# Performance work log

Hardware: AMD Instinct MI355X
Metric: run time of the kernel (lower is better)

The kernel has to match this reference:

```python
import jax, jax.numpy as jnp
import numpy as np

NEG_INF = -1e9  # stands in for the -inf diagonal mask of criss-cross attention
BN_EPS = 1e-5


def conv1x1(x, w, b=None):
    # x: [B,Cin,H,W], w: [Cout,Cin]
    y = jnp.einsum('bchw,oc->bohw', x, w)
    if b is not None:
        y = y + b[None, :, None, None]
    return y


def criss_cross(qf, kf, vf, q_w, q_b, k_w, k_b, v_w, v_b, gamma):
    # Criss-cross attention (CCNet): row + column affinity, joint softmax, aggregate.
    B, C, H, W = vf.shape
    q = conv1x1(qf, q_w, q_b)  # [B,Ci,H,W]
    k = conv1x1(kf, k_w, k_b)  # [B,Ci,H,W]
    v = conv1x1(vf, v_w, v_b)  # [B,C,H,W]
    # column-wise (along H) energy, with -inf on the self position (h == h')
    eH = jnp.einsum('bchw,bcHw->bhwH', q, k)
    eH = eH + NEG_INF * jnp.eye(H, dtype=eH.dtype)[:, None, :]  # [H,1,H] broadcasts over w
    # row-wise (along W) energy
    eW = jnp.einsum('bchw,bchW->bhwW', q, k)
    att = jax.nn.softmax(jnp.concatenate([eH, eW], axis=-1), axis=-1)  # [B,H,W,H+W]
    aH, aW = att[..., :H], att[..., H:]
    outH = jnp.einsum('bcHw,bhwH->bchw', v, aH)
    outW = jnp.einsum('bchW,bhwW->bchw', v, aW)
    return gamma * (outH + outW) + vf


def batchnorm(x, scale, bias):
    # training-mode BN over (N,H,W)
    mean = x.mean(axis=(0, 2, 3), keepdims=True)
    var = x.var(axis=(0, 2, 3), keepdims=True)
    xh = (x - mean) * jax.lax.rsqrt(var + BN_EPS)
    return xh * scale[None, :, None, None] + bias[None, :, None, None]


def setup_inputs() -> dict:
    key = jax.random.key(0)
    ks = jax.random.split(key, 16)
    B, C, H, W = 8, 512, 96, 96
    Hh, Wh = 48, 48
    Cin = C // 2    # 256
    Ci = C // 16    # 32
    s = 0.02
    inp = {
        'low_feature': jax.random.normal(ks[0], (B, C, H, W), jnp.float32),
        'high_feature': jax.random.normal(ks[1], (B, C, Hh, Wh), jnp.float32),
        'conv1_w': jax.random.normal(ks[2], (Cin, C), jnp.float32) * s,
        'conv1_b': jnp.zeros((Cin,), jnp.float32),
        'conv2_w': jax.random.normal(ks[3], (Cin, C), jnp.float32) * s,
        'conv2_b': jnp.zeros((Cin,), jnp.float32),
        'q_w': jax.random.normal(ks[4], (Ci, Cin), jnp.float32) * s,
        'q_b': jnp.zeros((Ci,), jnp.float32),
        'k_w': jax.random.normal(ks[5], (Ci, Cin), jnp.float32) * s,
        'k_b': jnp.zeros((Ci,), jnp.float32),
        'v_w': jax.random.normal(ks[6], (Cin, Cin), jnp.float32) * s,
        'v_b': jnp.zeros((Cin,), jnp.float32),
        'gamma': jnp.array(0.1, jnp.float32),
        'bottleneck_w': jax.random.normal(ks[7], (C, Cin + C), jnp.float32) * s,
        'bn_scale': jnp.ones((C,), jnp.float32),
        'bn_bias': jnp.zeros((C,), jnp.float32),
    }
    return inp


def reference(low_feature, high_feature, conv1_w, conv1_b, conv2_w, conv2_b,
              q_w, q_b, k_w, k_b, v_w, v_b, gamma, bottleneck_w, bn_scale, bn_bias):
    B, C, H, W = low_feature.shape
    hf = jax.image.resize(high_feature, (B, high_feature.shape[1], H, W), method='bilinear')
    qf = conv1x1(low_feature, conv1_w, conv1_b)   # [B,C/2,H,W]
    vf = conv1x1(hf, conv2_w, conv2_b)            # [B,C/2,H,W]
    for _ in range(2):  # module applies the same attention twice
        vf = criss_cross(qf, vf, vf, q_w, q_b, k_w, k_b, v_w, v_b, gamma)
    cat = jnp.concatenate([vf, hf], axis=1)       # [B, C/2 + C, H, W]
    out = conv1x1(cat, bottleneck_w)              # bias=False
    out = batchnorm(out, bn_scale, bn_bias)
    return jax.nn.relu(out)
```

## Files before the change

kernel.cpp:

```cpp
#include <hip/hip_runtime.h>
#include <hip/hip_bf16.h>

typedef __hip_bfloat16 bf16;
typedef __attribute__((ext_vector_type(8))) short short8;
typedef __attribute__((ext_vector_type(4))) float f32x4;

constexpr int kHW = 96 * 96;

__device__ __forceinline__ float b2f(bf16 x){ return __bfloat162float(x); }
__device__ __forceinline__ bf16  f2b(float x){ return __float2bfloat16(x); }

__global__ void k_zero(float* __restrict__ p){
  int i = blockIdx.x*256 + threadIdx.x;
  if (i < 1024) p[i] = 0.0f;
}

__global__ void k_cvt(const float* __restrict__ s, bf16* __restrict__ d, int n){
  int i = blockIdx.x*256 + threadIdx.x;
  if (i < n) d[i] = f2b(s[i]);
}

__global__ __launch_bounds__(256) void k_upsample(const float* __restrict__ hi,
                                                  bf16* __restrict__ hf_t){
  int y = blockIdx.x, b = blockIdx.y, t = threadIdx.x;
  int j = y >> 1;
  int j0, j1; float wy0, wy1;
  if ((y & 1) == 0){ j0 = j - 1; if (j0 < 0) j0 = 0; j1 = j; wy0 = 0.25f; wy1 = 0.75f; }
  else             { j0 = j; j1 = j + 1; if (j1 > 47) j1 = 47; wy0 = 0.75f; wy1 = 0.25f; }
  __shared__ __align__(16) float sm[2][128][49];
  for (int c0 = 0; c0 < 512; c0 += 128){
    for (int e = t; e < 2*128*48; e += 256){
      int cl = e / 96; int r = e % 96; int jj = r / 48; int i = r % 48;
      int row = jj ? j1 : j0;
      sm[jj][cl][i] = hi[(((size_t)b*512 + c0 + cl)*48 + row)*48 + i];
    }
    __syncthreads();
    for (int e = t; e < 96*128; e += 256){
      int x = e >> 7; int cl = e & 127;
      int i = x >> 1; int i0, i1; float wx0, wx1;
      if ((x & 1) == 0){ i0 = i - 1; if (i0 < 0) i0 = 0; i1 = i; wx0 = 0.25f; wx1 = 0.75f; }
      else             { i0 = i; i1 = i + 1; if (i1 > 47) i1 = 47; wx0 = 0.75f; wx1 = 0.25f; }
      float v = wy0*(wx0*sm[0][cl][i0] + wx1*sm[0][cl][i1])
              + wy1*(wx0*sm[1][cl][i0] + wx1*sm[1][cl][i1]);
      hf_t[(((size_t)b*96 + x)*96 + y)*512 + c0 + cl] = f2b(v);
    }
    __syncthreads();
  }
}

__global__ void k_qqw(const float* __restrict__ q_w, const float* __restrict__ c1_w,
                      float* __restrict__ qq_w){
  int gid = blockIdx.x*256 + threadIdx.x;
  int o = gid >> 9, c = gid & 511;
  float acc = 0.f;
  for (int k = 0; k < 256; k++) acc += q_w[o*256 + k] * c1_w[k*512 + c];
  qq_w[gid] = acc;
}
__global__ void k_qqb(const float* __restrict__ q_w, const float* __restrict__ c1_b,
                      const float* __restrict__ q_b, float* __restrict__ qq_b){
  int o = threadIdx.x; if (o >= 32) return;
  float acc = q_b[o];
  for (int k = 0; k < 256; k++) acc += q_w[o*256 + k] * c1_b[k];
  qq_b[o] = acc;
}

__global__ __launch_bounds__(256) void k_mfma_gemm(const bf16* __restrict__ A,
                                                   const bf16* __restrict__ Wb,
                                                   const float* __restrict__ bias,
                                                   bf16* __restrict__ out,
                                                   int K, int O){
  int b = blockIdx.z, n0 = blockIdx.x*128, o0 = blockIdx.y*128;
  int t = threadIdx.x, lane = t & 63, wv = t >> 6;
  int m_off = (wv & 1)*64, o_off = (wv >> 1)*64;
  int lm = lane & 15, lk = lane >> 4;
  __shared__ __align__(16) bf16 As[128*40];
  __shared__ __align__(16) bf16 Ws[128*40];
  f32x4 acc[4][4] = {};
  const bf16* Ab = A + (size_t)b*kHW*K;
  for (int c0 = 0; c0 < K; c0 += 32){
    for (int e = t; e < 512; e += 256){
      int nl = e >> 2, p = e & 3;
      *(uint4*)&As[nl*40 + p*8] = *(const uint4*)&Ab[(size_t)(n0+nl)*K + c0 + p*8];
    }
    for (int e = t; e < 512; e += 256){
      int ol = e >> 2, p = e & 3;
      *(uint4*)&Ws[ol*40 + p*8] = *(const uint4*)&Wb[(size_t)(o0+ol)*K + c0 + p*8];
    }
    __syncthreads();
    short8 af[4], bfr[4];
    #pragma unroll
    for (int i = 0; i < 4; i++){
      af[i]  = *(const short8*)&As[(m_off + i*16 + lm)*40 + lk*8];
      bfr[i] = *(const short8*)&Ws[(o_off + i*16 + lm)*40 + lk*8];
    }
    #pragma unroll
    for (int i = 0; i < 4; i++)
      #pragma unroll
      for (int j = 0; j < 4; j++)
        acc[i][j] = __builtin_amdgcn_mfma_f32_16x16x32_bf16(af[i], bfr[j], acc[i][j], 0, 0, 0);
    __syncthreads();
  }
  #pragma unroll
  for (int j = 0; j < 4; j++){
    int oc = o0 + o_off + j*16 + lm;
    float bs = bias ? bias[oc] : 0.0f;
    #pragma unroll
    for (int i = 0; i < 4; i++){
      int rbase = n0 + m_off + i*16 + lk*4;
      #pragma unroll
      for (int r = 0; r < 4; r++)
        out[((size_t)b*kHW + rbase + r)*(size_t)O + oc] = f2b(acc[i][j][r] + bs);
    }
  }
}

__global__ __launch_bounds__(256) void k_bneck_mfma(const bf16* __restrict__ vf,
                                                    const bf16* __restrict__ hf,
                                                    const bf16* __restrict__ Wb,
                                                    bf16* __restrict__ out){
  int b = blockIdx.z, n0 = blockIdx.x*128, o0 = blockIdx.y*128;
  int t = threadIdx.x, lane = t & 63, wv = t >> 6;
  int m_off = (wv & 1)*64, o_off = (wv >> 1)*64;
  int lm = lane & 15, lk = lane >> 4;
  __shared__ __align__(16) bf16 As[128*40];
  __shared__ __align__(16) bf16 Ws[128*40];
  f32x4 acc[4][4] = {};
  for (int c0 = 0; c0 < 768; c0 += 32){
    const bf16* src; int strd, cc;
    if (c0 < 256){ src = vf + (size_t)b*kHW*256; strd = 256; cc = c0; }
    else         { src = hf + (size_t)b*kHW*512; strd = 512; cc = c0 - 256; }
    for (int e = t; e < 512; e += 256){
      int nl = e >> 2, p = e & 3;
      *(uint4*)&As[nl*40 + p*8] = *(const uint4*)&src[(size_t)(n0+nl)*strd + cc + p*8];
    }
    for (int e = t; e < 512; e += 256){
      int ol = e >> 2, p = e & 3;
      *(uint4*)&Ws[ol*40 + p*8] = *(const uint4*)&Wb[(size_t)(o0+ol)*768 + c0 + p*8];
    }
    __syncthreads();
    short8 af[4], bfr[4];
    #pragma unroll
    for (int i = 0; i < 4; i++){
      af[i]  = *(const short8*)&As[(m_off + i*16 + lm)*40 + lk*8];
      bfr[i] = *(const short8*)&Ws[(o_off + i*16 + lm)*40 + lk*8];
    }
    #pragma unroll
    for (int i = 0; i < 4; i++)
      #pragma unroll
      for (int j = 0; j < 4; j++)
        acc[i][j] = __builtin_amdgcn_mfma_f32_16x16x32_bf16(af[i], bfr[j], acc[i][j], 0, 0, 0);
    __syncthreads();
  }
  #pragma unroll
  for (int j = 0; j < 4; j++){
    int oc = o0 + o_off + j*16 + lm;
    #pragma unroll
    for (int i = 0; i < 4; i++){
      int rbase = n0 + m_off + i*16 + lk*4;
      #pragma unroll
      for (int r = 0; r < 4; r++)
        out[((size_t)b*kHW + rbase + r)*512 + oc] = f2b(acc[i][j][r]);
    }
  }
}

__global__ __launch_bounds__(256) void k_stats(const bf16* __restrict__ bt,
                                               float* __restrict__ s1,
                                               float* __restrict__ s2){
  int n0 = blockIdx.x*256, b = blockIdx.y, t = threadIdx.x;
  __shared__ float l1[512];
  __shared__ float l2[512];
  for (int e = t; e < 512; e += 256){ l1[e] = 0.f; l2[e] = 0.f; }
  __syncthreads();
  int og = (t & 63)*8;
  int r0 = t >> 6;
  float a1[8] = {}, a2[8] = {};
  for (int r = r0; r < 256; r += 4){
    const bf16* p = bt + ((size_t)b*kHW + n0 + r)*512 + og;
    uint4 d = *(const uint4*)p;
    const unsigned short* us = (const unsigned short*)&d;
    #pragma unroll
    for (int j = 0; j < 8; j++){
      float v = __uint_as_float(((unsigned)us[j]) << 16);
      a1[j] += v; a2[j] += v*v;
    }
  }
  #pragma unroll
  for (int j = 0; j < 8; j++){
    atomicAdd(&l1[og + j], a1[j]);
    atomicAdd(&l2[og + j], a2[j]);
  }
  __syncthreads();
  for (int e = t; e < 512; e += 256){
    atomicAdd(&s1[e], l1[e]);
    atomicAdd(&s2[e], l2[e]);
  }
}

__global__ __launch_bounds__(256) void k_qlow(const float* __restrict__ low,
                                              const float* __restrict__ qq_w,
                                              const float* __restrict__ qq_b,
                                              bf16* __restrict__ q_t){
  int h = blockIdx.x, b = blockIdx.y, t = threadIdx.x;
  int tw = t % 32, to = t / 32;
  __shared__ __align__(16) float Al[64][98];
  __shared__ __align__(16) float Wl[64][36];
  float acc[3][4] = {};
  for (int c0 = 0; c0 < 512; c0 += 64){
    for (int e = t; e < 64*96; e += 256){
      int cl = e / 96, x = e % 96;
      Al[cl][x] = low[(((size_t)b*512 + c0 + cl)*96 + h)*96 + x];
    }
    for (int e = t; e < 32*64; e += 256){
      int o = e >> 6, k = e & 63;
      Wl[k][o] = qq_w[(size_t)o*512 + c0 + k];
    }
    __syncthreads();
    #pragma unroll 4
    for (int k = 0; k < 64; k++){
      float a_[3];
      #pragma unroll
      for (int i = 0; i < 3; i++) a_[i] = Al[k][tw*3 + i];
      float4 wv = *(const float4*)&Wl[k][to*4];
      float w_[4] = {wv.x, wv.y, wv.z, wv.w};
      #pragma unroll
      for (int i = 0; i < 3; i++)
        #pragma unroll
        for (int jj = 0; jj < 4; jj++) acc[i][jj] += a_[i]*w_[jj];
    }
    __syncthreads();
  }
  #pragma unroll
  for (int i = 0; i < 3; i++){
    int x = tw*3 + i;
    size_t base = (((size_t)b*96 + x)*96 + h)*32 + to*4;
    #pragma unroll
    for (int jj = 0; jj < 4; jj++) q_t[base + jj] = f2b(acc[i][jj] + qq_b[to*4 + jj]);
  }
}

template<int BN, int OT>
__global__ __launch_bounds__(256) void k_gemm_bb(const bf16* __restrict__ A,
                                                 const float* __restrict__ Wt,
                                                 const float* __restrict__ bias,
                                                 bf16* __restrict__ out,
                                                 int Cin, int O){
  constexpr int TN = BN/4;
  int b = blockIdx.z, n0 = blockIdx.x*BN, o0 = blockIdx.y*OT, t = threadIdx.x;
  int tn = t % TN, to = t / TN;
  __shared__ __align__(16) float As[32][BN+4];
  __shared__ __align__(16) float Ws[32][OT+4];
  float acc[4][4] = {};
  const bf16* Ab = A + (size_t)b*kHW*Cin;
  for (int c0 = 0; c0 < Cin; c0 += 32){
    for (int e = t; e < BN*32; e += 256){
      int nl = e >> 5, kk = e & 31;
      As[kk][nl] = b2f(Ab[(size_t)(n0+nl)*Cin + c0 + kk]);
    }
    for (int e = t; e < OT*32; e += 256){
      int ol = e >> 5, kk = e & 31;
      Ws[kk][ol] = Wt[(size_t)(o0+ol)*Cin + c0 + kk];
    }
    __syncthreads();
    #pragma unroll
    for (int kk = 0; kk < 32; kk++){
      float4 av = *(const float4*)&As[kk][tn*4];
      float4 wv = *(const float4*)&Ws[kk][to*4];
      float a_[4] = {av.x, av.y, av.z, av.w};
      float w_[4] = {wv.x, wv.y, wv.z, wv.w};
      #pragma unroll
      for (int i = 0; i < 4; i++)
        #pragma unroll
        for (int jj = 0; jj < 4; jj++) acc[i][jj] += a_[i]*w_[jj];
    }
    __syncthreads();
  }
  #pragma unroll
  for (int i = 0; i < 4; i++){
    size_t base = ((size_t)b*kHW + n0 + tn*4 + i)*(size_t)O + o0 + to*4;
    #pragma unroll
    for (int jj = 0; jj < 4; jj++) out[base + jj] = f2b(acc[i][jj] + bias[o0 + to*4 + jj]);
  }
}

__global__ __launch_bounds__(256) void k_eH(const bf16* __restrict__ q_t,
                                            const bf16* __restrict__ k_t,
                                            bf16* __restrict__ att){
  int w = blockIdx.x, b = blockIdx.y, t = threadIdx.x;
  __shared__ float Qs[96][33];
  __shared__ float Ks[96][33];
  const bf16* Qp = q_t + (((size_t)b*96 + w)*96)*32;
  const bf16* Kp = k_t + (((size_t)b*96 + w)*96)*32;
  for (int e = t; e < 3072; e += 256){ Qs[e>>5][e&31] = b2f(Qp[e]); Ks[e>>5][e&31] = b2f(Kp[e]); }
  __syncthreads();
  int tj = t % 16, th = t / 16;
  float acc[6][6] = {};
  #pragma unroll 4
  for (int c = 0; c < 32; c++){
    float qa[6], kb[6];
    #pragma unroll
    for (int i = 0; i < 6; i++) qa[i] = Qs[th*6 + i][c];
    #pragma unroll
    for (int jj = 0; jj < 6; jj++) kb[jj] = Ks[tj*6 + jj][c];
    #pragma unroll
    for (int i = 0; i < 6; i++)
      #pragma unroll
      for (int jj = 0; jj < 6; jj++) acc[i][jj] += qa[i]*kb[jj];
  }
  #pragma unroll
  for (int i = 0; i < 6; i++){
    int h = th*6 + i;
    size_t base = (((size_t)b*96 + h)*96 + w)*192;
    #pragma unroll
    for (int jj = 0; jj < 6; jj++){
      int jg = tj*6 + jj;
      float e = acc[i][jj];
      if (jg == h) e += -1000000000.0f;
      att[base + jg] = f2b(e);
    }
  }
}

__global__ __launch_bounds__(256) void k_eW(const bf16* __restrict__ q_t,
                                            const bf16* __restrict__ k_t,
                                            bf16* __restrict__ att){
  int h = blockIdx.x, b = blockIdx.y, t = threadIdx.x;
  __shared__ float Qs[96][33];
  __shared__ float Ks[96][33];
  for (int e = t; e < 3072; e += 256){
    int wl = e >> 5, c = e & 31;
    size_t idx = (((size_t)b*96 + wl)*96 + h)*32 + c;
    Qs[wl][c] = b2f(q_t[idx]);
    Ks[wl][c] = b2f(k_t[idx]);
  }
  __syncthreads();
  int tj = t % 16, tw = t / 16;
  float acc[6][6] = {};
  #pragma unroll 4
  for (int c = 0; c < 32; c++){
    float qa[6], kb[6];
    #pragma unroll
    for (int i = 0; i < 6; i++) qa[i] = Qs[tw*6 + i][c];
    #pragma unroll
    for (int jj = 0; jj < 6; jj++) kb[jj] = Ks[tj*6 + jj][c];
    #pragma unroll
    for (int i = 0; i < 6; i++)
      #pragma unroll
      for (int jj = 0; jj < 6; jj++) acc[i][jj] += qa[i]*kb[jj];
  }
  #pragma unroll
  for (int i = 0; i < 6; i++){
    int wl = tw*6 + i;
    size_t base = (((size_t)b*96 + h)*96 + wl)*192 + 96;
    #pragma unroll
    for (int jj = 0; jj < 6; jj++) att[base + tj*6 + jj] = f2b(acc[i][jj]);
  }
}

__global__ __launch_bounds__(256) void k_softmax(bf16* __restrict__ att){
  int t = threadIdx.x;
  int row = blockIdx.x*4 + (t >> 6);
  int lane = t & 63;
  size_t base = (size_t)row * 192;
  float x0 = b2f(att[base + lane]);
  float x1 = b2f(att[base + 64 + lane]);
  float x2 = b2f(att[base + 128 + lane]);
  float m = fmaxf(x0, fmaxf(x1, x2));
  #pragma unroll
  for (int off = 32; off; off >>= 1) m = fmaxf(m, __shfl_xor(m, off));
  float e0 = __expf(x0 - m), e1 = __expf(x1 - m), e2 = __expf(x2 - m);
  float s = e0 + e1 + e2;
  #pragma unroll
  for (int off = 32; off; off >>= 1) s += __shfl_xor(s, off);
  float inv = 1.0f / s;
  att[base + lane]       = f2b(e0 * inv);
  att[base + 64 + lane]  = f2b(e1 * inv);
  att[base + 128 + lane] = f2b(e2 * inv);
}

__global__ __launch_bounds__(256) void k_outH_mfma(const bf16* __restrict__ att,
                                                   const bf16* __restrict__ v_t,
                                                   bf16* __restrict__ accb){
  int w = blockIdx.x, b = blockIdx.y, t = threadIdx.x;
  int lane = t & 63, wv = t >> 6;
  int m_off = (wv & 1)*48, o_off = (wv >> 1)*128;
  int lm = lane & 15, lk = lane >> 4;
  __shared__ __align__(16) bf16 As[96*36];
  __shared__ __align__(16) bf16 Vt[256*36];
  f32x4 acc[3][8] = {};
  const bf16* Vb = v_t + ((size_t)b*96 + w)*96*256;
  for (int j0 = 0; j0 < 96; j0 += 32){
    for (int e = t; e < 384; e += 256){
      int h = e >> 2, p = e & 3;
      *(uint4*)&As[h*36 + p*8] =
        *(const uint4*)&att[(((size_t)b*96 + h)*96 + w)*192 + j0 + p*8];
    }
    for (int e = t; e < 512; e += 256){
      int jj2 = (e & 15)*2, cg = e >> 4;
      const bf16* p = Vb + (size_t)(j0 + jj2)*256 + cg*8;
      uint4 a0 = *(const uint4*)p;
      uint4 a1 = *(const uint4*)(p + 256);
      const unsigned short* u0 = (const unsigned short*)&a0;
      const unsigned short* u1 = (const unsigned short*)&a1;
      #pragma unroll
      for (int u = 0; u < 8; u++){
        ushort2 pr; pr.x = u0[u]; pr.y = u1[u];
        *(ushort2*)&Vt[(cg*8 + u)*36 + jj2] = pr;
      }
    }
    __syncthreads();
    short8 af[3], bfr[8];
    #pragma unroll
    for (int i = 0; i < 3; i++)
      af[i] = *(const short8*)&As[(m_off + i*16 + lm)*36 + lk*8];
    #pragma unroll
    for (int j = 0; j < 8; j++)
      bfr[j] = *(const short8*)&Vt[(o_off + j*16 + lm)*36 + lk*8];
    #pragma unroll
    for (int i = 0; i < 3; i++)
      #pragma unroll
      for (int j = 0; j < 8; j++)
        acc[i][j] = __builtin_amdgcn_mfma_f32_16x16x32_bf16(af[i], bfr[j], acc[i][j], 0, 0, 0);
    __syncthreads();
  }
  #pragma unroll
  for (int j = 0; j < 8; j++){
    int c = o_off + j*16 + lm;
    #pragma unroll
    for (int i = 0; i < 3; i++){
      int hbase = m_off + i*16 + lk*4;
      #pragma unroll
      for (int r = 0; r < 4; r++)
        accb[(((size_t)b*96 + w)*96 + hbase + r)*256 + c] = f2b(acc[i][j][r]);
    }
  }
}

__global__ __launch_bounds__(256) void k_outW_mfma(const bf16* __restrict__ att,
                                                   const bf16* __restrict__ v_t,
                                                   const bf16* __restrict__ accb,
                                                   const float* __restrict__ gamma_p,
                                                   bf16* __restrict__ vf_t){
  int h = blockIdx.x, b = blockIdx.y, t = threadIdx.x;
  int lane = t & 63, wv = t >> 6;
  int m_off = (wv & 1)*48, o_off = (wv >> 1)*128;
  int lm = lane & 15, lk = lane >> 4;
  __shared__ __align__(16) bf16 As[96*36];
  __shared__ __align__(16) bf16 Vt[256*36];
  f32x4 acc[3][8] = {};
  for (int j0 = 0; j0 < 96; j0 += 32){
    for (int e = t; e < 384; e += 256){
      int wl = e >> 2, p = e & 3;
      *(uint4*)&As[wl*36 + p*8] =
        *(const uint4*)&att[(((size_t)b*96 + h)*96 + wl)*192 + 96 + j0 + p*8];
    }
    for (int e = t; e < 512; e += 256){
      int jj2 = (e & 15)*2, cg = e >> 4;
      const bf16* p = v_t + (((size_t)b*96 + j0 + jj2)*96 + h)*256 + cg*8;
      uint4 a0 = *(const uint4*)p;
      uint4 a1 = *(const uint4*)(p + 96*256);
      const unsigned short* u0 = (const unsigned short*)&a0;
      const unsigned short* u1 = (const unsigned short*)&a1;
      #pragma unroll
      for (int u = 0; u < 8; u++){
        ushort2 pr; pr.x = u0[u]; pr.y = u1[u];
        *(ushort2*)&Vt[(cg*8 + u)*36 + jj2] = pr;
      }
    }
    __syncthreads();
    short8 af[3], bfr[8];
    #pragma unroll
    for (int i = 0; i < 3; i++)
      af[i] = *(const short8*)&As[(m_off + i*16 + lm)*36 + lk*8];
    #pragma unroll
    for (int j = 0; j < 8; j++)
      bfr[j] = *(const short8*)&Vt[(o_off + j*16 + lm)*36 + lk*8];
    #pragma unroll
    for (int i = 0; i < 3; i++)
      #pragma unroll
      for (int j = 0; j < 8; j++)
        acc[i][j] = __builtin_amdgcn_mfma_f32_16x16x32_bf16(af[i], bfr[j], acc[i][j], 0, 0, 0);
    __syncthreads();
  }
  float g = gamma_p[0];
  #pragma unroll
  for (int j = 0; j < 8; j++){
    int c = o_off + j*16 + lm;
    #pragma unroll
    for (int i = 0; i < 3; i++){
      int wbase = m_off + i*16 + lk*4;
      #pragma unroll
      for (int r = 0; r < 4; r++){
        size_t idx = (((size_t)b*96 + wbase + r)*96 + h)*256 + c;
        vf_t[idx] = f2b(b2f(vf_t[idx]) + g*(acc[i][j][r] + b2f(accb[idx])));
      }
    }
  }
}

__global__ void k_bnprep(const float* __restrict__ s1, const float* __restrict__ s2,
                         const float* __restrict__ sc, const float* __restrict__ bi,
                         float2* __restrict__ ab){
  int co = blockIdx.x*256 + threadIdx.x;
  if (co >= 512) return;
  const float N = 73728.0f;
  float mean = s1[co] / N;
  float var  = s2[co] / N - mean*mean;
  if (var < 0.f) var = 0.f;
  float a = rsqrtf(var + 1e-5f) * sc[co];
  ab[co] = make_float2(a, bi[co] - mean*a);
}

__global__ __launch_bounds__(256) void k_bnout(const bf16* __restrict__ bt,
                                               const float2* __restrict__ ab,
                                               float* __restrict__ out){
  int w0 = blockIdx.x*32, h = blockIdx.y, b = blockIdx.z, t = threadIdx.x;
  __shared__ float Tl[32][33];
  for (int co0 = 0; co0 < 512; co0 += 32){
    for (int e = t; e < 1024; e += 256){
      int wl = e >> 5, co = e & 31;
      Tl[wl][co] = b2f(bt[(((size_t)b*96 + w0 + wl)*96 + h)*512 + co0 + co]);
    }
    __syncthreads();
    for (int e = t; e < 1024; e += 256){
      int co = e >> 5, wl = e & 31;
      float2 s = ab[co0 + co];
      float v = fmaxf(Tl[wl][co]*s.x + s.y, 0.0f);
      out[(((size_t)b*512 + co0 + co)*96 + h)*96 + w0 + wl] = v;
    }
    __syncthreads();
  }
}

extern "C" void kernel_launch(void* const* d_in, const int* in_sizes, int n_in,
                              void* d_out, int out_size, void* d_ws, size_t ws_size,
                              hipStream_t stream){
  (void)in_sizes; (void)n_in; (void)out_size; (void)ws_size;
  const float* low   = (const float*)d_in[0];
  const float* high  = (const float*)d_in[1];
  const float* c1w   = (const float*)d_in[2];
  const float* c1b   = (const float*)d_in[3];
  const float* c2w   = (const float*)d_in[4];
  const float* c2b   = (const float*)d_in[5];
  const float* qw    = (const float*)d_in[6];
  const float* qb    = (const float*)d_in[7];
  const float* kw    = (const float*)d_in[8];
  const float* kb    = (const float*)d_in[9];
  const float* vw    = (const float*)d_in[10];
  const float* vb    = (const float*)d_in[11];
  const float* gamma = (const float*)d_in[12];
  const float* bw    = (const float*)d_in[13];
  const float* bns   = (const float*)d_in[14];
  const float* bnb   = (const float*)d_in[15];
  float* out = (float*)d_out;

  char* wsb = (char*)d_ws;
  bf16*   hf_t = (bf16*) (wsb + 0);
  bf16*   vf_t = (bf16*) (wsb + 75497472);
  bf16*   q_t  = (bf16*) (wsb + 113246208);
  float*  qq_w = (float*)(wsb + 117964800);
  float*  qq_b = (float*)(wsb + 118030336);
  float*  s1   = (float*)(wsb + 118030464);
  float*  s2   = (float*)(wsb + 118032512);
  float2* ab   = (float2*)(wsb + 118034560);
  bf16*   wbb  = (bf16*) (wsb + 118038656);
  bf16*   wc2  = (bf16*) (wsb + 118825088);
  bf16*   wv   = (bf16*) (wsb + 119087232);
  bf16*   v_t  = (bf16*) (wsb + 119218304);
  bf16*   att  = (bf16*) (wsb + 156967040);
  bf16*   accb = (bf16*) (wsb + 185278592);
  bf16*   k_t  = (bf16*) (wsb + 185278592);
  bf16*   bt   = (bf16*) (wsb + 119218304);

  k_zero<<<4, 256, 0, stream>>>(s1);
  k_cvt<<<1536, 256, 0, stream>>>(bw,  wbb, 393216);
  k_cvt<<<512,  256, 0, stream>>>(c2w, wc2, 131072);
  k_cvt<<<256,  256, 0, stream>>>(vw,  wv,  65536);
  k_upsample<<<dim3(96, 8), 256, 0, stream>>>(high, hf_t);
  k_qqw<<<64, 256, 0, stream>>>(qw, c1w, qq_w);
  k_qqb<<<1, 64, 0, stream>>>(qw, c1b, qb, qq_b);
  k_mfma_gemm<<<dim3(72, 2, 8), 256, 0, stream>>>(hf_t, wc2, c2b, vf_t, 512, 256);
  k_qlow<<<dim3(96, 8), 256, 0, stream>>>(low, qq_w, qq_b, q_t);

  for (int r = 0; r < 2; r++){
    k_gemm_bb<128, 32><<<dim3(72, 1, 8), 256, 0, stream>>>(vf_t, kw, kb, k_t, 256, 32);
    k_mfma_gemm<<<dim3(72, 2, 8), 256, 0, stream>>>(vf_t, wv, vb, v_t, 256, 256);
    k_eH<<<dim3(96, 8), 256, 0, stream>>>(q_t, k_t, att);
    k_eW<<<dim3(96, 8), 256, 0, stream>>>(q_t, k_t, att);
    k_softmax<<<18432, 256, 0, stream>>>(att);
    k_outH_mfma<<<dim3(96, 8), 256, 0, stream>>>(att, v_t, accb);
    k_outW_mfma<<<dim3(96, 8), 256, 0, stream>>>(att, v_t, accb, gamma, vf_t);
  }

  k_bneck_mfma<<<dim3(72, 4, 8), 256, 0, stream>>>(vf_t, hf_t, wbb, bt);
  k_stats<<<dim3(36, 8), 256, 0, stream>>>(bt, s1, s2);
  k_bnprep<<<2, 256, 0, stream>>>(s1, s2, bns, bnb, ab);
  k_bnout<<<dim3(3, 96, 8), 256, 0, stream>>>(bt, ab, out);
}
```

Measured before the change: 1.156 ms.

## Double-buffer MFMA GEMM tiles and fuse BN statistics into bottleneck GEMM

Both MFMA GEMM kernels now stage K-tiles in two LDS buffers, holding the next tile's global loads in registers while the current tile's MFMAs run. This cuts one barrier per iteration and hides load latency. The BN sum and sum-of-squares reduction moves into the bottleneck GEMM epilogue through shared then global atomics, so the separate stats pass that re-read the bf16 output goes away. The stats are now taken from the fp32 accumulators rather than the rounded bf16 values, and LDS use doubles.

```diff
diff --git a/kernel.cpp b/kernel.cpp
--- a/kernel.cpp
+++ b/kernel.cpp
@@ -9,6 +9,7 @@
 
 __device__ __forceinline__ float b2f(bf16 x){ return __bfloat162float(x); }
 __device__ __forceinline__ bf16  f2b(float x){ return __float2bfloat16(x); }
+
 
 __global__ void k_zero(float* __restrict__ p){
   int i = blockIdx.x*256 + threadIdx.x;
@@ -73,32 +74,50 @@
   int t = threadIdx.x, lane = t & 63, wv = t >> 6;
   int m_off = (wv & 1)*64, o_off = (wv >> 1)*64;
   int lm = lane & 15, lk = lane >> 4;
-  __shared__ __align__(16) bf16 As[128*40];
-  __shared__ __align__(16) bf16 Ws[128*40];
+  __shared__ __align__(16) bf16 As[2][128*40];
+  __shared__ __align__(16) bf16 Ws[2][128*40];
   f32x4 acc[4][4] = {};
   const bf16* Ab = A + (size_t)b*kHW*K;
-  for (int c0 = 0; c0 < K; c0 += 32){
-    for (int e = t; e < 512; e += 256){
-      int nl = e >> 2, p = e & 3;
-      *(uint4*)&As[nl*40 + p*8] = *(const uint4*)&Ab[(size_t)(n0+nl)*K + c0 + p*8];
-    }
-    for (int e = t; e < 512; e += 256){
-      int ol = e >> 2, p = e & 3;
-      *(uint4*)&Ws[ol*40 + p*8] = *(const uint4*)&Wb[(size_t)(o0+ol)*K + c0 + p*8];
+  int nl0 = t >> 2, p0 = (t & 3)*8;
+  uint4 pa0, pa1, pw0, pw1;
+  pa0 = *(const uint4*)&Ab[(size_t)(n0+nl0)*K + p0];
+  pa1 = *(const uint4*)&Ab[(size_t)(n0+nl0+64)*K + p0];
+  pw0 = *(const uint4*)&Wb[(size_t)(o0+nl0)*K + p0];
+  pw1 = *(const uint4*)&Wb[(size_t)(o0+nl0+64)*K + p0];
+  *(uint4*)&As[0][nl0*40 + p0]      = pa0;
+  *(uint4*)&As[0][(nl0+64)*40 + p0] = pa1;
+  *(uint4*)&Ws[0][nl0*40 + p0]      = pw0;
+  *(uint4*)&Ws[0][(nl0+64)*40 + p0] = pw1;
+  int cur = 0;
+  int NS = K >> 5;
+  for (int s = 0; s < NS; s++){
+    if (s+1 < NS){
+      int c0 = (s+1)*32;
+      pa0 = *(const uint4*)&Ab[(size_t)(n0+nl0)*K + c0 + p0];
+      pa1 = *(const uint4*)&Ab[(size_t)(n0+nl0+64)*K + c0 + p0];
+      pw0 = *(const uint4*)&Wb[(size_t)(o0+nl0)*K + c0 + p0];
+      pw1 = *(const uint4*)&Wb[(size_t)(o0+nl0+64)*K + c0 + p0];
     }
     __syncthreads();
     short8 af[4], bfr[4];
     #pragma unroll
     for (int i = 0; i < 4; i++){
-      af[i]  = *(const short8*)&As[(m_off + i*16 + lm)*40 + lk*8];
-      bfr[i] = *(const short8*)&Ws[(o_off + i*16 + lm)*40 + lk*8];
+      af[i]  = *(const short8*)&As[cur][(m_off + i*16 + lm)*40 + lk*8];
+      bfr[i] = *(const short8*)&Ws[cur][(o_off + i*16 + lm)*40 + lk*8];
     }
     #pragma unroll
     for (int i = 0; i < 4; i++)
       #pragma unroll
       for (int j = 0; j < 4; j++)
         acc[i][j] = __builtin_amdgcn_mfma_f32_16x16x32_bf16(af[i], bfr[j], acc[i][j], 0, 0, 0);
-    __syncthreads();
+    if (s+1 < NS){
+      int nx = cur ^ 1;
+      *(uint4*)&As[nx][nl0*40 + p0]      = pa0;
+      *(uint4*)&As[nx][(nl0+64)*40 + p0] = pa1;
+      *(uint4*)&Ws[nx][nl0*40 + p0]      = pw0;
+      *(uint4*)&Ws[nx][(nl0+64)*40 + p0] = pw1;
+      cur = nx;
+    }
   }
   #pragma unroll
   for (int j = 0; j < 4; j++){
@@ -117,83 +136,89 @@
 __global__ __launch_bounds__(256) void k_bneck_mfma(const bf16* __restrict__ vf,
                                                     const bf16* __restrict__ hf,
                                                     const bf16* __restrict__ Wb,
-                                                    bf16* __restrict__ out){
+                                                    bf16* __restrict__ out,
+                                                    float* __restrict__ s1,
+                                                    float* __restrict__ s2){
   int b = blockIdx.z, n0 = blockIdx.x*128, o0 = blockIdx.y*128;
   int t = threadIdx.x, lane = t & 63, wv = t >> 6;
   int m_off = (wv & 1)*64, o_off = (wv >> 1)*64;
   int lm = lane & 15, lk = lane >> 4;
-  __shared__ __align__(16) bf16 As[128*40];
-  __shared__ __align__(16) bf16 Ws[128*40];
+  __shared__ __align__(16) bf16 As[2][128*40];
+  __shared__ __align__(16) bf16 Ws[2][128*40];
+  __shared__ float l1[128];
+  __shared__ float l2[128];
+  if (t < 128){ l1[t] = 0.f; l2[t] = 0.f; }
   f32x4 acc[4][4] = {};
-  for (int c0 = 0; c0 < 768; c0 += 32){
-    const bf16* src; int strd, cc;
-    if (c0 < 256){ src = vf + (size_t)b*kHW*256; strd = 256; cc = c0; }
-    else         { src = hf + (size_t)b*kHW*512; strd = 512; cc = c0 - 256; }
-    for (int e = t; e < 512; e += 256){
-      int nl = e >> 2, p = e & 3;
-      *(uint4*)&As[nl*40 + p*8] = *(const uint4*)&src[(size_t)(n0+nl)*strd + cc + p*8];
-    }
-    for (int e = t; e < 512; e += 256){
-      int ol = e >> 2, p = e & 3;
-      *(uint4*)&Ws[ol*40 + p*8] = *(const uint4*)&Wb[(size_t)(o0+ol)*768 + c0 + p*8];
+  int nl0 = t >> 2, p0 = (t & 3)*8;
+  const bf16* vfb = vf + (size_t)b*kHW*256;
+  const bf16* hfb = hf + (size_t)b*kHW*512;
+  uint4 pa0, pa1, pw0, pw1;
+  pa0 = *(const uint4*)&vfb[(size_t)(n0+nl0)*256 + p0];
+  pa1 = *(const uint4*)&vfb[(size_t)(n0+nl0+64)*256 + p0];
+  pw0 = *(const uint4*)&Wb[(size_t)(o0+nl0)*768 + p0];
+  pw1 = *(const uint4*)&Wb[(size_t)(o0+nl0+64)*768 + p0];
+  *(uint4*)&As[0][nl0*40 + p0]      = pa0;
+  *(uint4*)&As[0][(nl0+64)*40 + p0] = pa1;
+  *(uint4*)&Ws[0][nl0*40 + p0]      = pw0;
+  *(uint4*)&Ws[0][(nl0+64)*40 + p0] = pw1;
+  int cur = 0;
+  for (int s = 0; s < 24; s++){
+    if (s+1 < 24){
+      int c0 = (s+1)*32;
+      if (c0 < 256){
+        pa0 = *(const uint4*)&vfb[(size_t)(n0+nl0)*256 + c0 + p0];
+        pa1 = *(const uint4*)&vfb[(size_t)(n0+nl0+64)*256 + c0 + p0];
+      } else {
+        int cc = c0 - 256;
+        pa0 = *(const uint4*)&hfb[(size_t)(n0+nl0)*512 + cc + p0];
+        pa1 = *(const uint4*)&hfb[(size_t)(n0+nl0+64)*512 + cc + p0];
+      }
+      pw0 = *(const uint4*)&Wb[(size_t)(o0+nl0)*768 + c0 + p0];
+      pw1 = *(const uint4*)&Wb[(size_t)(o0+nl0+64)*768 + c0 + p0];
     }
     __syncthreads();
     short8 af[4], bfr[4];
     #pragma unroll
     for (int i = 0; i < 4; i++){
-      af[i]  = *(const short8*)&As[(m_off + i*16 + lm)*40 + lk*8];
-      bfr[i] = *(const short8*)&Ws[(o_off + i*16 + lm)*40 + lk*8];
+      af[i]  = *(const short8*)&As[cur][(m_off + i*16 + lm)*40 + lk*8];
+      bfr[i] = *(const short8*)&Ws[cur][(o_off + i*16 + lm)*40 + lk*8];
     }
     #pragma unroll
     for (int i = 0; i < 4; i++)
       #pragma unroll
       for (int j = 0; j < 4; j++)
         acc[i][j] = __builtin_amdgcn_mfma_f32_16x16x32_bf16(af[i], bfr[j], acc[i][j], 0, 0, 0);
-    __syncthreads();
+    if (s+1 < 24){
+      int nx = cur ^ 1;
+      *(uint4*)&As[nx][nl0*40 + p0]      = pa0;
+      *(uint4*)&As[nx][(nl0+64)*40 + p0] = pa1;
+      *(uint4*)&Ws[nx][nl0*40 + p0]      = pw0;
+      *(uint4*)&Ws[nx][(nl0+64)*40 + p0] = pw1;
+      cur = nx;
+    }
   }
   #pragma unroll
   for (int j = 0; j < 4; j++){
     int oc = o0 + o_off + j*16 + lm;
+    float p1 = 0.f, p2 = 0.f;
     #pragma unroll
     for (int i = 0; i < 4; i++){
       int rbase = n0 + m_off + i*16 + lk*4;
       #pragma unroll
-      for (int r = 0; r < 4; r++)
-        out[((size_t)b*kHW + rbase + r)*512 + oc] = f2b(acc[i][j][r]);
-    }
-  }
-}
-
-__global__ __launch_bounds__(256) void k_stats(const bf16* __restrict__ bt,
-                                               float* __restrict__ s1,
-                                               float* __restrict__ s2){
-  int n0 = blockIdx.x*256, b = blockIdx.y, t = threadIdx.x;
-  __shared__ float l1[512];
-  __shared__ float l2[512];
-  for (int e = t; e < 512; e += 256){ l1[e] = 0.f; l2[e] = 0.f; }
+      for (int r = 0; r < 4; r++){
+        float v = acc[i][j][r];
+        p1 += v; p2 += v*v;
+        out[((size_t)b*kHW + rbase + r)*512 + oc] = f2b(v);
+      }
+    }
+    int cl = o_off + j*16 + lm;
+    atomicAdd(&l1[cl], p1);
+    atomicAdd(&l2[cl], p2);
+  }
   __syncthreads();
-  int og = (t & 63)*8;
-  int r0 = t >> 6;
-  float a1[8] = {}, a2[8] = {};
-  for (int r = r0; r < 256; r += 4){
-    const bf16* p = bt + ((size_t)b*kHW + n0 + r)*512 + og;
-    uint4 d = *(const uint4*)p;
-    const unsigned short* us = (const unsigned short*)&d;
-    #pragma unroll
-    for (int j = 0; j < 8; j++){
-      float v = __uint_as_float(((unsigned)us[j]) << 16);
-      a1[j] += v; a2[j] += v*v;
-    }
-  }
-  #pragma unroll
-  for (int j = 0; j < 8; j++){
-    atomicAdd(&l1[og + j], a1[j]);
-    atomicAdd(&l2[og + j], a2[j]);
-  }
-  __syncthreads();
-  for (int e = t; e < 512; e += 256){
-    atomicAdd(&s1[e], l1[e]);
-    atomicAdd(&s2[e], l2[e]);
+  if (t < 128){
+    atomicAdd(&s1[o0 + t], l1[t]);
+    atomicAdd(&s2[o0 + t], l2[t]);
   }
 }
 
@@ -592,8 +617,7 @@
     k_outW_mfma<<<dim3(96, 8), 256, 0, stream>>>(att, v_t, accb, gamma, vf_t);
   }
 
-  k_bneck_mfma<<<dim3(72, 4, 8), 256, 0, stream>>>(vf_t, hf_t, wbb, bt);
-  k_stats<<<dim3(36, 8), 256, 0, stream>>>(bt, s1, s2);
+  k_bneck_mfma<<<dim3(72, 4, 8), 256, 0, stream>>>(vf_t, hf_t, wbb, bt, s1, s2);
   k_bnprep<<<2, 256, 0, stream>>>(s1, s2, bns, bnb, ab);
   k_bnout<<<dim3(3, 96, 8), 256, 0, stream>>>(bt, ab, out);
 }
```

New measurement: 1.063 ms. -8.0%, faster.
